# Performance work log

Hardware: AMD Instinct MI355X
Metric: run time of the kernel (lower is better)

Reference implementation:

```python
import jax, jax.numpy as jnp
import numpy as np

B = 1024
E = 512
NUM_HEADS = 8
EPS = 1e-5  # torch LayerNorm default


def _mha(x, w_qkv, b_qkv, w_o, b_o):
    """torch nn.MultiheadAttention (batch_first, self-attn, no dropout).
    x: [N, S, E]; w_qkv: [3E, E]; w_o: [E, E]."""
    N, S, Ex = x.shape
    H = NUM_HEADS
    D = Ex // H
    qkv = x @ w_qkv.T + b_qkv                      # [N, S, 3E]
    q, k, v = jnp.split(qkv, 3, axis=-1)
    q = q.reshape(N, S, H, D).transpose(0, 2, 1, 3)  # [N, H, S, D]
    k = k.reshape(N, S, H, D).transpose(0, 2, 1, 3)
    v = v.reshape(N, S, H, D).transpose(0, 2, 1, 3)
    scores = jnp.einsum('nhqd,nhkd->nhqk', q, k) * (D ** -0.5)
    attn = jax.nn.softmax(scores, axis=-1)
    out = jnp.einsum('nhqk,nhkd->nhqd', attn, v)
    out = out.transpose(0, 2, 1, 3).reshape(N, S, Ex)
    return out @ w_o.T + b_o


def _box_perm(g):
    """Permute 9x9 grid so each 3x3 box becomes a contiguous row of 9.
    This permutation is its own inverse. g: [B, 9, 9, E]."""
    Bx = g.shape[0]
    return (g.reshape(Bx, 3, 3, 3, 3, E)
             .transpose(0, 1, 3, 2, 4, 5)
             .reshape(Bx, 9, 9, E))


def setup_inputs() -> dict:
    key = jax.random.key(0)
    ks = jax.random.split(key, 16)
    s = 0.02
    inp = {'x': jax.random.normal(ks[0], (B, 81, E), jnp.float32)}
    for i, p in enumerate(['row', 'col', 'box']):
        inp[p + '_wqkv'] = jax.random.normal(ks[1 + 2 * i], (3 * E, E), jnp.float32) * s
        inp[p + '_bqkv'] = jnp.zeros((3 * E,), jnp.float32)
        inp[p + '_wo'] = jax.random.normal(ks[2 + 2 * i], (E, E), jnp.float32) * s
        inp[p + '_bo'] = jnp.zeros((E,), jnp.float32)
    inp['w1'] = jax.random.normal(ks[7], (2 * E, 3 * E), jnp.float32) * s
    inp['b1'] = jnp.zeros((2 * E,), jnp.float32)
    inp['w2'] = jax.random.normal(ks[8], (E, 2 * E), jnp.float32) * s
    inp['b2'] = jnp.zeros((E,), jnp.float32)
    inp['gamma'] = jnp.ones((E,), jnp.float32)
    inp['beta'] = jnp.zeros((E,), jnp.float32)
    return inp


def reference(x, row_wqkv, row_bqkv, row_wo, row_bo,
              col_wqkv, col_bqkv, col_wo, col_bo,
              box_wqkv, box_bqkv, box_wo, box_bo,
              w1, b1, w2, b2, gamma, beta):
    Bx = x.shape[0]
    # Row attention: rows are already contiguous groups of 9.
    row_out = _mha(x.reshape(Bx * 9, 9, E), row_wqkv, row_bqkv, row_wo, row_bo)
    row_out = row_out.reshape(Bx, 81, E)
    # Column attention: transpose grid so columns are contiguous.
    col_x = x.reshape(Bx, 9, 9, E).transpose(0, 2, 1, 3).reshape(Bx * 9, 9, E)
    col_out = _mha(col_x, col_wqkv, col_bqkv, col_wo, col_bo)
    col_out = col_out.reshape(Bx, 9, 9, E).transpose(0, 2, 1, 3).reshape(Bx, 81, E)
    # Box attention: permute grid so each 3x3 box is contiguous.
    box_x = _box_perm(x.reshape(Bx, 9, 9, E)).reshape(Bx * 9, 9, E)
    box_out = _mha(box_x, box_wqkv, box_bqkv, box_wo, box_bo)
    box_out = _box_perm(box_out.reshape(Bx, 9, 9, E)).reshape(Bx, 81, E)
    # Constraint mixer MLP.
    combined = jnp.concatenate([row_out, col_out, box_out], axis=-1)  # [B,81,3E]
    h = jax.nn.gelu(combined @ w1.T + b1, approximate=False)
    mixed = h @ w2.T + b2
    # Residual + LayerNorm.
    y = x + mixed
    mu = jnp.mean(y, axis=-1, keepdims=True)
    var = jnp.var(y, axis=-1, keepdims=True)
    return (y - mu) * jax.lax.rsqrt(var + EPS) * gamma + beta
```

## Files before the change

### kernel.cpp

```cpp
#include <hip/hip_runtime.h>
#include <hip/hip_bf16.h>
#include <math.h>

typedef __hip_bfloat16 bf16;
typedef __attribute__((ext_vector_type(8))) short s8v;
typedef __attribute__((ext_vector_type(4))) short s4v;
typedef __attribute__((ext_vector_type(4))) float f4v;

static __device__ __forceinline__ float bfs2f(short s) {
    return __uint_as_float(((unsigned)(unsigned short)s) << 16);
}
static __device__ __forceinline__ short f2bfs(float f) {
    __hip_bfloat16 h = __float2bfloat16(f);
    return *reinterpret_cast<short*>(&h);
}

__global__ __launch_bounds__(256)
void cvt_f32_bf16(const float* __restrict__ in, bf16* __restrict__ out, long n4)
{
    const long i = (long)blockIdx.x * 256 + threadIdx.x;
    if (i >= n4) return;
    const float4 v = reinterpret_cast<const float4*>(in)[i];
    s4v o;
    o[0] = f2bfs(v.x); o[1] = f2bfs(v.y); o[2] = f2bfs(v.z); o[3] = f2bfs(v.w);
    reinterpret_cast<s4v*>(out)[i] = o;
}

__global__ __launch_bounds__(256)
void cvt_t_f32_bf16(const float* __restrict__ in, bf16* __restrict__ out,
                    int R, int C)
{
    __shared__ float t[32][33];
    const int bx = blockIdx.x * 32;
    const int by = blockIdx.y * 32;
    const int tx = threadIdx.x & 31;
    const int ty = threadIdx.x >> 5;
#pragma unroll
    for (int r = ty; r < 32; r += 8)
        t[r][tx] = in[(long)(by + r) * C + bx + tx];
    __syncthreads();
#pragma unroll
    for (int r = ty; r < 32; r += 8)
        out[(long)(bx + r) * R + by + tx] = __float2bfloat16(t[tx][r]);
}

__global__ __launch_bounds__(256)
void fold_b1(const float* __restrict__ w1, const float* __restrict__ bo0,
             const float* __restrict__ bo1, const float* __restrict__ bo2,
             const float* __restrict__ b1, float* __restrict__ b1p)
{
    const int m = blockIdx.x * 256 + threadIdx.x;
    float s = b1[m];
    const float* w = w1 + (long)m * 1536;
    for (int k = 0; k < 512; ++k) s += w[k]        * bo0[k];
    for (int k = 0; k < 512; ++k) s += w[512 + k]  * bo1[k];
    for (int k = 0; k < 512; ++k) s += w[1024 + k] * bo2[k];
    b1p[m] = s;
}

template<int ACT>
__global__ __launch_bounds__(512, 2)
void gemm256(const bf16* __restrict__ A, const bf16* __restrict__ B,
             const float* __restrict__ bias, bf16* __restrict__ C,
             int K, int lda, int ldc, int coff)
{
    __shared__ __align__(16) bf16 sA[2][256 * 64];
    __shared__ __align__(16) bf16 sB[2][256 * 64];
    const int tid  = threadIdx.x;
    const int lane = tid & 63;
    const int wid  = tid >> 6;
    const int nwg  = gridDim.x * gridDim.y;
    const int orig = blockIdx.x + gridDim.x * blockIdx.y;
    const int q = nwg >> 3, r = nwg & 7, xcd = orig & 7;
    const int sb = (xcd < r ? xcd * (q + 1) : r * (q + 1) + (xcd - r) * q) + (orig >> 3);
    const int bCol = sb % gridDim.x;
    const int bRow = sb / gridDim.x;

    const int wr  = (wid >> 2) * 128;
    const int wc  = (wid & 3) * 64;
    const int fr  = lane & 15;
    const int hi4 = lane >> 4;
    const int rx  = fr & 7;

    f4v acc[8][4];
#pragma unroll
    for (int i = 0; i < 8; ++i)
#pragma unroll
        for (int j = 0; j < 4; ++j) acc[i][j] = (f4v)(0.0f);

    const int srow = tid >> 3;
    const int scol = ((tid & 7) ^ (srow & 7)) * 8;
    const bf16* Abase = A + (long)(bRow * 256 + srow) * lda + scol;
    const bf16* Bbase = B + (long)(bCol * 256 + srow) * K + scol;

#define GL16(src, dst)                                                          \
    __builtin_amdgcn_global_load_lds(                                           \
        (const __attribute__((address_space(1))) unsigned int*)(src),           \
        (__attribute__((address_space(3))) unsigned int*)(dst), 16, 0, 0)

#define STAGE_A(h, tt, bc) do {                                                 \
    const bf16* g_ = Abase + (long)(h) * 128 * lda + (long)(tt) * 64;           \
    char* d_ = (char*)sA[bc] + (h) * 16384 + tid * 16;                          \
    GL16(g_, d_); GL16(g_ + 64 * (long)lda, d_ + 8192); } while (0)

#define STAGE_B(h, tt, bc) do {                                                 \
    const bf16* g_ = Bbase + (long)(h) * 128 * K + (long)(tt) * 64;             \
    char* d_ = (char*)sB[bc] + (h) * 16384 + tid * 16;                          \
    GL16(g_, d_); GL16(g_ + 64 * (long)K, d_ + 8192); } while (0)

    const int nk = K >> 6;

    STAGE_A(0, 0, 0); STAGE_A(1, 0, 0);
    STAGE_B(0, 0, 0); STAGE_B(1, 0, 0);
    STAGE_B(0, 1, 1); STAGE_B(1, 1, 1);
    asm volatile("s_waitcnt vmcnt(4)" ::: "memory");
    __builtin_amdgcn_s_barrier();
    __builtin_amdgcn_sched_barrier(0);

    for (int t = 0; t < nk; ++t) {
        const int c = t & 1;
        const char* sAc = (const char*)sA[c];
        const char* sBc = (const char*)sB[c];
        s8v bfr[4][2];
#pragma unroll
        for (int p = 0; p < 4; ++p) {
            s8v afr[2][2];
#pragma unroll
            for (int m2 = 0; m2 < 2; ++m2)
#pragma unroll
                for (int kk = 0; kk < 2; ++kk)
                    afr[m2][kk] = *(const s8v*)(sAc
                        + (wr + (2 * p + m2) * 16 + fr) * 128
                        + (((kk * 4 + hi4) ^ rx) << 4));
            if (p == 0) {
#pragma unroll
                for (int ni = 0; ni < 4; ++ni)
#pragma unroll
                    for (int kk = 0; kk < 2; ++kk)
                        bfr[ni][kk] = *(const s8v*)(sBc
                            + (wc + ni * 16 + fr) * 128
                            + (((kk * 4 + hi4) ^ rx) << 4));
            }
            if (p == 0 && t + 1 < nk) STAGE_A(0, t + 1, c ^ 1);
            if (p == 1 && t + 1 < nk) STAGE_A(1, t + 1, c ^ 1);
            if (p == 2 && t + 2 < nk) STAGE_B(0, t + 2, c);
            if (p == 3 && t + 2 < nk) STAGE_B(1, t + 2, c);

            __builtin_amdgcn_s_barrier();
            asm volatile("s_waitcnt lgkmcnt(0)" ::: "memory");
            __builtin_amdgcn_sched_barrier(0);
            __builtin_amdgcn_s_setprio(1);
#pragma unroll
            for (int kk = 0; kk < 2; ++kk)
#pragma unroll
                for (int m2 = 0; m2 < 2; ++m2)
#pragma unroll
                    for (int ni = 0; ni < 4; ++ni)
                        acc[2 * p + m2][ni] = __builtin_amdgcn_mfma_f32_16x16x32_bf16(
                            afr[m2][kk], bfr[ni][kk], acc[2 * p + m2][ni], 0, 0, 0);
            __builtin_amdgcn_s_setprio(0);
            __builtin_amdgcn_sched_barrier(0);
            if (p == 3) {
                if (t + 2 < nk) {
                    asm volatile("s_waitcnt vmcnt(4)" ::: "memory");
                } else if (t + 1 < nk) {
                    asm volatile("s_waitcnt vmcnt(0)" ::: "memory");
                }
            }
            __builtin_amdgcn_s_barrier();
            __builtin_amdgcn_sched_barrier(0);
        }
    }
#undef STAGE_A
#undef STAGE_B
#undef GL16

    const int frow = hi4 * 4;
    const long rowBase = (long)bRow * 256 + wr;
    const int  colBase = bCol * 256 + wc;
#pragma unroll
    for (int ni = 0; ni < 4; ++ni) {
        const int col = colBase + ni * 16 + fr;
        const float bi = bias ? bias[coff + col] : 0.0f;
#pragma unroll
        for (int mi = 0; mi < 8; ++mi) {
#pragma unroll
            for (int j = 0; j < 4; ++j) {
                float v = acc[mi][ni][j] + bi;
                if (ACT == 1) {
                    const float u = v * (0.7978845608f + 0.0356774081f * v * v);
                    const float tnh = 1.0f - 2.0f / (__expf(2.0f * u) + 1.0f);
                    v = 0.5f * v * (1.0f + tnh);
                }
                const long rr = rowBase + mi * 16 + frow + j;
                C[rr * (long)ldc + coff + col] = __float2bfloat16(v);
            }
        }
    }
}

__global__ __launch_bounds__(256)
void attn9(const bf16* __restrict__ qkv, bf16* __restrict__ outg,
           long chunk_base)
{
    __shared__ __align__(16) bf16 sQKV[9 * 1536];
    __shared__ float sP[8 * 81];
    __shared__ int sTok[9];
    const int tid = threadIdx.x;
    const int branch = blockIdx.y;
    const int bx = blockIdx.x;
    const int s = (bx & 7) * (2304 >> 3) + (bx >> 3);
    const int b = s / 9, g = s % 9;

    if (tid < 9) {
        const int p = tid;
        int cell;
        if (branch == 0)      cell = g * 9 + p;
        else if (branch == 1) cell = p * 9 + g;
        else                  cell = ((g / 3) * 3 + p / 3) * 9 + (g % 3) * 3 + (p % 3);
        sTok[p] = b * 81 + cell;
    }
    __syncthreads();

    const long brOff = (long)branch * 1536;
    for (int c = tid; c < 1728; c += 256) {
        const int p = c / 192;
        const int off = (c - p * 192) * 8;
        *(s8v*)(&sQKV[p * 1536 + off]) =
            *(const s8v*)(&qkv[(long)sTok[p] * 4608 + brOff + off]);
    }
    __syncthreads();

    for (int t = tid; t < 648; t += 256) {
        const int h = t / 81;
        const int r = t - h * 81;
        const int i = r / 9, j = r - (r / 9) * 9;
        const bf16* qp = &sQKV[i * 1536 + h * 64];
        const bf16* kp = &sQKV[j * 1536 + 512 + h * 64];
        float accd = 0.0f;
#pragma unroll
        for (int dc = 0; dc < 8; ++dc) {
            s8v qv = *(const s8v*)(qp + dc * 8);
            s8v kv = *(const s8v*)(kp + dc * 8);
#pragma unroll
            for (int e2 = 0; e2 < 8; ++e2)
                accd += bfs2f(qv[e2]) * bfs2f(kv[e2]);
        }
        sP[t] = accd * 0.125f;
    }
    __syncthreads();

    if (tid < 72) {
        float* row = &sP[tid * 9];
        float m = row[0];
#pragma unroll
        for (int j = 1; j < 9; ++j) m = fmaxf(m, row[j]);
        float sum = 0.f, e[9];
#pragma unroll
        for (int j = 0; j < 9; ++j) { e[j] = expf(row[j] - m); sum += e[j]; }
        const float inv = 1.0f / sum;
#pragma unroll
        for (int j = 0; j < 9; ++j) row[j] = e[j] * inv;
    }
    __syncthreads();

    for (int t = tid; t < 576; t += 256) {
        const int i = t >> 6;
        const int c8 = (t & 63) * 8;
        const int h = (t & 63) >> 3;
        const float* prow = &sP[h * 81 + i * 9];
        float accv[8];
#pragma unroll
        for (int q2 = 0; q2 < 8; ++q2) accv[q2] = 0.f;
#pragma unroll
        for (int j = 0; j < 9; ++j) {
            const float p = prow[j];
            s8v vv = *(const s8v*)(&sQKV[j * 1536 + 1024 + c8]);
#pragma unroll
            for (int q2 = 0; q2 < 8; ++q2)
                accv[q2] += p * bfs2f(vv[q2]);
        }
        s8v ov;
#pragma unroll
        for (int q2 = 0; q2 < 8; ++q2) ov[q2] = f2bfs(accv[q2]);
        *(s8v*)(&outg[(chunk_base + sTok[i]) * 1536 + branch * 512 + c8]) = ov;
    }
}

__global__ __launch_bounds__(256)
void ln_res(const float* __restrict__ x, const bf16* __restrict__ mixed,
            const float* __restrict__ gamma, const float* __restrict__ beta,
            float* __restrict__ out)
{
    const int tid = threadIdx.x;
    const int lane = tid & 63;
    const long row = (long)blockIdx.x * 4 + (tid >> 6);
    const long base = row * 512 + lane * 8;
    const float4 x0 = *(const float4*)(&x[base]);
    const float4 x1 = *(const float4*)(&x[base + 4]);
    const s8v mv = *(const s8v*)(&mixed[base]);
    float y[8];
    y[0] = x0.x + bfs2f(mv[0]); y[1] = x0.y + bfs2f(mv[1]);
    y[2] = x0.z + bfs2f(mv[2]); y[3] = x0.w + bfs2f(mv[3]);
    y[4] = x1.x + bfs2f(mv[4]); y[5] = x1.y + bfs2f(mv[5]);
    y[6] = x1.z + bfs2f(mv[6]); y[7] = x1.w + bfs2f(mv[7]);
    float sum = 0.f, sq = 0.f;
#pragma unroll
    for (int j = 0; j < 8; ++j) { sum += y[j]; sq += y[j] * y[j]; }
#pragma unroll
    for (int o = 32; o > 0; o >>= 1) {
        sum += __shfl_xor(sum, o, 64);
        sq  += __shfl_xor(sq, o, 64);
    }
    const float mean = sum * (1.f / 512.f);
    const float inv = rsqrtf(sq * (1.f / 512.f) - mean * mean + 1e-5f);
    const float4 g0 = *(const float4*)(&gamma[lane * 8]);
    const float4 g1 = *(const float4*)(&gamma[lane * 8 + 4]);
    const float4 b0 = *(const float4*)(&beta[lane * 8]);
    const float4 b1 = *(const float4*)(&beta[lane * 8 + 4]);
    float4 o0, o1;
    o0.x = (y[0] - mean) * inv * g0.x + b0.x;
    o0.y = (y[1] - mean) * inv * g0.y + b0.y;
    o0.z = (y[2] - mean) * inv * g0.z + b0.z;
    o0.w = (y[3] - mean) * inv * g0.w + b0.w;
    o1.x = (y[4] - mean) * inv * g1.x + b1.x;
    o1.y = (y[5] - mean) * inv * g1.y + b1.y;
    o1.z = (y[6] - mean) * inv * g1.z + b1.z;
    o1.w = (y[7] - mean) * inv * g1.w + b1.w;
    *(float4*)(&out[base]) = o0;
    *(float4*)(&out[base + 4]) = o1;
}

extern "C" void kernel_launch(void* const* d_in, const int* in_sizes, int n_in,
                              void* d_out, int out_size, void* d_ws, size_t ws_size,
                              hipStream_t stream)
{
    (void)in_sizes; (void)n_in; (void)out_size; (void)ws_size;
    const float* x     = (const float*)d_in[0];
    const float* w1f   = (const float*)d_in[13];
    const float* b1f   = (const float*)d_in[14];
    const float* b2f   = (const float*)d_in[16];
    const float* gamma = (const float*)d_in[17];
    const float* beta  = (const float*)d_in[18];

    char* ws = (char*)d_ws;
    bf16* attnall   = (bf16*)(ws);
    bf16* mixed     = (bf16*)(ws);
    char* R         = ws + 254803968LL;
    bf16* qkv3chunk = (bf16*)(R);
    bf16* xb        = (bf16*)(R + 191102976LL);
    bf16* h         = (bf16*)(R);
    char* wb        = ws + 530841600LL;
    long off = 0;
    bf16* wqkv3_b = (bf16*)(wb + off); off += 4718592;
    bf16* woT_b[3];
    for (int i = 0; i < 3; ++i) { woT_b[i] = (bf16*)(wb + off); off += 524288; }
    bf16* w1_b  = (bf16*)(wb + off); off += 3145728;
    bf16* w2_b  = (bf16*)(wb + off); off += 1048576;
    bf16* Wp    = (bf16*)(wb + off); off += 3145728;
    float* b1p  = (float*)(wb + off); off += 4096;
    float* bqkv3 = (float*)(wb + off); off += 18432;

    const dim3 blk(256, 1, 1);
    const dim3 blk512(512, 1, 1);

    cvt_f32_bf16<<<dim3(41472), blk, 0, stream>>>(x, xb, 10616832L);
    for (int i = 0; i < 3; ++i) {
        cvt_f32_bf16<<<dim3(768), blk, 0, stream>>>(
            (const float*)d_in[1 + i * 4], wqkv3_b + (long)i * 786432, 196608L);
        cvt_t_f32_bf16<<<dim3(16, 16), blk, 0, stream>>>(
            (const float*)d_in[3 + i * 4], woT_b[i], 512, 512);
        hipMemcpyAsync(bqkv3 + i * 1536, d_in[2 + i * 4], 1536 * sizeof(float),
                       hipMemcpyDeviceToDevice, stream);
    }
    cvt_f32_bf16<<<dim3(1536), blk, 0, stream>>>(w1f, w1_b, 393216L);
    cvt_f32_bf16<<<dim3(512), blk, 0, stream>>>((const float*)d_in[15], w2_b, 131072L);

    fold_b1<<<dim3(4), blk, 0, stream>>>(w1f, (const float*)d_in[4],
                                         (const float*)d_in[8], (const float*)d_in[12],
                                         b1f, b1p);

    for (int br = 0; br < 3; ++br)
        gemm256<0><<<dim3(2, 4), blk512, 0, stream>>>(
            w1_b + br * 512, woT_b[br], nullptr, Wp, 512, 1536, 1536, br * 512);

    const long ROWS_C = 20736;
    for (int c = 0; c < 4; ++c) {
        const bf16* xA = xb + c * ROWS_C * 512;
        gemm256<0><<<dim3(18, 81), blk512, 0, stream>>>(
            xA, wqkv3_b, bqkv3, qkv3chunk, 512, 512, 4608, 0);
        attn9<<<dim3(2304, 3), blk, 0, stream>>>(qkv3chunk, attnall, c * ROWS_C);
    }
    gemm256<1><<<dim3(4, 324), blk512, 0, stream>>>(attnall, Wp, b1p, h, 1536, 1536, 1024, 0);
    gemm256<0><<<dim3(2, 324), blk512, 0, stream>>>(h, w2_b, b2f, mixed, 1024, 1024, 512, 0);
    ln_res<<<dim3(20736), blk, 0, stream>>>(x, mixed, gamma, beta, (float*)d_out);
}
```

Before: 1.727 ms.

## Restructure GEMM K-loop into two phases with fewer barriers and explicit waits

Each K step of the bf16 MFMA GEMM main loop now runs in two phases instead of four, each covering half the M fragments. The per-phase barriers, lgkmcnt waits and sched_barriers are removed, so the compiler schedules the LDS reads and MFMAs freely. The intent is to cut synchronisation overhead and let LDS loads overlap with matrix math. The trade-off is more live fragment registers and reliance on compiler-inserted waits, which could raise register pressure or add hazards around the async global-to-LDS staging.

```diff
diff --git a/kernel.cpp b/kernel.cpp
--- a/kernel.cpp
+++ b/kernel.cpp
@@ -108,6 +108,9 @@
     char* d_ = (char*)sB[bc] + (h) * 16384 + tid * 16;                          \
     GL16(g_, d_); GL16(g_ + 64 * (long)K, d_ + 8192); } while (0)
 
+#define LDSW(base, row, kk)                                                     \
+    (*(const s8v*)((base) + (row) * 128 + ((((kk) * 4 + hi4) ^ rx) << 4)))
+
     const int nk = K >> 6;
 
     STAGE_A(0, 0, 0); STAGE_A(1, 0, 0);
@@ -122,58 +125,74 @@
         const char* sAc = (const char*)sA[c];
         const char* sBc = (const char*)sB[c];
         s8v bfr[4][2];
-#pragma unroll
-        for (int p = 0; p < 4; ++p) {
-            s8v afr[2][2];
+
+        {
+            s8v af0[2][2], af1[2][2];
 #pragma unroll
             for (int m2 = 0; m2 < 2; ++m2)
 #pragma unroll
+                for (int kk = 0; kk < 2; ++kk) {
+                    af0[m2][kk] = LDSW(sAc, wr + m2 * 16 + fr, kk);
+                    af1[m2][kk] = LDSW(sAc, wr + (2 + m2) * 16 + fr, kk);
+                }
+#pragma unroll
+            for (int ni = 0; ni < 4; ++ni)
+#pragma unroll
                 for (int kk = 0; kk < 2; ++kk)
-                    afr[m2][kk] = *(const s8v*)(sAc
-                        + (wr + (2 * p + m2) * 16 + fr) * 128
-                        + (((kk * 4 + hi4) ^ rx) << 4));
-            if (p == 0) {
-#pragma unroll
-                for (int ni = 0; ni < 4; ++ni)
-#pragma unroll
-                    for (int kk = 0; kk < 2; ++kk)
-                        bfr[ni][kk] = *(const s8v*)(sBc
-                            + (wc + ni * 16 + fr) * 128
-                            + (((kk * 4 + hi4) ^ rx) << 4));
-            }
-            if (p == 0 && t + 1 < nk) STAGE_A(0, t + 1, c ^ 1);
-            if (p == 1 && t + 1 < nk) STAGE_A(1, t + 1, c ^ 1);
-            if (p == 2 && t + 2 < nk) STAGE_B(0, t + 2, c);
-            if (p == 3 && t + 2 < nk) STAGE_B(1, t + 2, c);
-
-            __builtin_amdgcn_s_barrier();
-            asm volatile("s_waitcnt lgkmcnt(0)" ::: "memory");
-            __builtin_amdgcn_sched_barrier(0);
+                    bfr[ni][kk] = LDSW(sBc, wc + ni * 16 + fr, kk);
+            if (t + 1 < nk) { STAGE_A(0, t + 1, c ^ 1); STAGE_A(1, t + 1, c ^ 1); }
             __builtin_amdgcn_s_setprio(1);
 #pragma unroll
             for (int kk = 0; kk < 2; ++kk)
 #pragma unroll
                 for (int m2 = 0; m2 < 2; ++m2)
 #pragma unroll
-                    for (int ni = 0; ni < 4; ++ni)
-                        acc[2 * p + m2][ni] = __builtin_amdgcn_mfma_f32_16x16x32_bf16(
-                            afr[m2][kk], bfr[ni][kk], acc[2 * p + m2][ni], 0, 0, 0);
+                    for (int ni = 0; ni < 4; ++ni) {
+                        acc[m2][ni] = __builtin_amdgcn_mfma_f32_16x16x32_bf16(
+                            af0[m2][kk], bfr[ni][kk], acc[m2][ni], 0, 0, 0);
+                        acc[2 + m2][ni] = __builtin_amdgcn_mfma_f32_16x16x32_bf16(
+                            af1[m2][kk], bfr[ni][kk], acc[2 + m2][ni], 0, 0, 0);
+                    }
             __builtin_amdgcn_s_setprio(0);
-            __builtin_amdgcn_sched_barrier(0);
-            if (p == 3) {
-                if (t + 2 < nk) {
-                    asm volatile("s_waitcnt vmcnt(4)" ::: "memory");
-                } else if (t + 1 < nk) {
-                    asm volatile("s_waitcnt vmcnt(0)" ::: "memory");
+        }
+        __builtin_amdgcn_s_barrier();
+
+        {
+            s8v af0[2][2], af1[2][2];
+#pragma unroll
+            for (int m2 = 0; m2 < 2; ++m2)
+#pragma unroll
+                for (int kk = 0; kk < 2; ++kk) {
+                    af0[m2][kk] = LDSW(sAc, wr + (4 + m2) * 16 + fr, kk);
+                    af1[m2][kk] = LDSW(sAc, wr + (6 + m2) * 16 + fr, kk);
                 }
-            }
-            __builtin_amdgcn_s_barrier();
-            __builtin_amdgcn_sched_barrier(0);
-        }
+            if (t + 2 < nk) { STAGE_B(0, t + 2, c); STAGE_B(1, t + 2, c); }
+            __builtin_amdgcn_s_setprio(1);
+#pragma unroll
+            for (int kk = 0; kk < 2; ++kk)
+#pragma unroll
+                for (int m2 = 0; m2 < 2; ++m2)
+#pragma unroll
+                    for (int ni = 0; ni < 4; ++ni) {
+                        acc[4 + m2][ni] = __builtin_amdgcn_mfma_f32_16x16x32_bf16(
+                            af0[m2][kk], bfr[ni][kk], acc[4 + m2][ni], 0, 0, 0);
+                        acc[6 + m2][ni] = __builtin_amdgcn_mfma_f32_16x16x32_bf16(
+                            af1[m2][kk], bfr[ni][kk], acc[6 + m2][ni], 0, 0, 0);
+                    }
+            __builtin_amdgcn_s_setprio(0);
+        }
+        if (t + 2 < nk) {
+            asm volatile("s_waitcnt vmcnt(4)" ::: "memory");
+        } else if (t + 1 < nk) {
+            asm volatile("s_waitcnt vmcnt(0)" ::: "memory");
+        }
+        __builtin_amdgcn_s_barrier();
+        __builtin_amdgcn_sched_barrier(0);
     }
 #undef STAGE_A
 #undef STAGE_B
 #undef GL16
+#undef LDSW
 
     const int frow = hi4 * 4;
     const long rowBase = (long)bRow * 256 + wr;
```

Result: faster. 1.564 ms (-9.4%).

## Simplify GEMM pipeline to one-ahead prefetch and stage epilogue through LDS

Applied to the files above, without the earlier changes.

Replaces the staggered four-phase main loop, which split the A and B prefetches across sub-phases with per-phase barriers, with a simpler loop. It prefetches the entire next K-tile at the top, computes all MFMAs for the current tile, then waits and synchronizes once per iteration. The epilogue now writes bias- and activation-adjusted results into shared memory per warp, then emits coalesced 16-byte row stores to global instead of scattered 2-byte stores. The fewer barriers and coalesced writes aim to cut sync and store overhead, but the loop loses the deeper B prefetch and the finer interleaving of loads with compute.

```diff
diff --git a/kernel.cpp b/kernel.cpp
--- a/kernel.cpp
+++ b/kernel.cpp
@@ -108,65 +108,56 @@
     char* d_ = (char*)sB[bc] + (h) * 16384 + tid * 16;                          \
     GL16(g_, d_); GL16(g_ + 64 * (long)K, d_ + 8192); } while (0)
 
+#define LDSW(base, row, kk)                                                     \
+    (*(const s8v*)((base) + (row) * 128 + ((((kk) * 4 + hi4) ^ rx) << 4)))
+
     const int nk = K >> 6;
 
     STAGE_A(0, 0, 0); STAGE_A(1, 0, 0);
     STAGE_B(0, 0, 0); STAGE_B(1, 0, 0);
-    STAGE_B(0, 1, 1); STAGE_B(1, 1, 1);
-    asm volatile("s_waitcnt vmcnt(4)" ::: "memory");
+    asm volatile("s_waitcnt vmcnt(0)" ::: "memory");
     __builtin_amdgcn_s_barrier();
-    __builtin_amdgcn_sched_barrier(0);
 
     for (int t = 0; t < nk; ++t) {
         const int c = t & 1;
         const char* sAc = (const char*)sA[c];
         const char* sBc = (const char*)sB[c];
+
+        if (t + 1 < nk) {
+            STAGE_A(0, t + 1, c ^ 1); STAGE_A(1, t + 1, c ^ 1);
+            STAGE_B(0, t + 1, c ^ 1); STAGE_B(1, t + 1, c ^ 1);
+        }
+
         s8v bfr[4][2];
 #pragma unroll
-        for (int p = 0; p < 4; ++p) {
-            s8v afr[2][2];
-#pragma unroll
-            for (int m2 = 0; m2 < 2; ++m2)
-#pragma unroll
-                for (int kk = 0; kk < 2; ++kk)
-                    afr[m2][kk] = *(const s8v*)(sAc
-                        + (wr + (2 * p + m2) * 16 + fr) * 128
-                        + (((kk * 4 + hi4) ^ rx) << 4));
-            if (p == 0) {
-#pragma unroll
-                for (int ni = 0; ni < 4; ++ni)
-#pragma unroll
-                    for (int kk = 0; kk < 2; ++kk)
-                        bfr[ni][kk] = *(const s8v*)(sBc
-                            + (wc + ni * 16 + fr) * 128
-                            + (((kk * 4 + hi4) ^ rx) << 4));
+        for (int ni = 0; ni < 4; ++ni)
+#pragma unroll
+            for (int kk = 0; kk < 2; ++kk)
+                bfr[ni][kk] = LDSW(sBc, wc + ni * 16 + fr, kk);
+
+#pragma unroll
+        for (int g = 0; g < 4; ++g) {
+            s8v a0[2], a1[2];
+#pragma unroll
+            for (int kk = 0; kk < 2; ++kk) {
+                a0[kk] = LDSW(sAc, wr + (2 * g) * 16 + fr, kk);
+                a1[kk] = LDSW(sAc, wr + (2 * g + 1) * 16 + fr, kk);
             }
-            if (p == 0 && t + 1 < nk) STAGE_A(0, t + 1, c ^ 1);
-            if (p == 1 && t + 1 < nk) STAGE_A(1, t + 1, c ^ 1);
-            if (p == 2 && t + 2 < nk) STAGE_B(0, t + 2, c);
-            if (p == 3 && t + 2 < nk) STAGE_B(1, t + 2, c);
-
-            __builtin_amdgcn_s_barrier();
-            asm volatile("s_waitcnt lgkmcnt(0)" ::: "memory");
-            __builtin_amdgcn_sched_barrier(0);
             __builtin_amdgcn_s_setprio(1);
 #pragma unroll
             for (int kk = 0; kk < 2; ++kk)
 #pragma unroll
-                for (int m2 = 0; m2 < 2; ++m2)
-#pragma unroll
-                    for (int ni = 0; ni < 4; ++ni)
-                        acc[2 * p + m2][ni] = __builtin_amdgcn_mfma_f32_16x16x32_bf16(
-                            afr[m2][kk], bfr[ni][kk], acc[2 * p + m2][ni], 0, 0, 0);
+                for (int ni = 0; ni < 4; ++ni) {
+                    acc[2 * g][ni] = __builtin_amdgcn_mfma_f32_16x16x32_bf16(
+                        a0[kk], bfr[ni][kk], acc[2 * g][ni], 0, 0, 0);
+                    acc[2 * g + 1][ni] = __builtin_amdgcn_mfma_f32_16x16x32_bf16(
+                        a1[kk], bfr[ni][kk], acc[2 * g + 1][ni], 0, 0, 0);
+                }
             __builtin_amdgcn_s_setprio(0);
-            __builtin_amdgcn_sched_barrier(0);
-            if (p == 3) {
-                if (t + 2 < nk) {
-                    asm volatile("s_waitcnt vmcnt(4)" ::: "memory");
-                } else if (t + 1 < nk) {
-                    asm volatile("s_waitcnt vmcnt(0)" ::: "memory");
-                }
-            }
+        }
+
+        if (t + 1 < nk) {
+            asm volatile("s_waitcnt vmcnt(0)" ::: "memory");
             __builtin_amdgcn_s_barrier();
             __builtin_amdgcn_sched_barrier(0);
         }
@@ -174,7 +165,11 @@
 #undef STAGE_A
 #undef STAGE_B
 #undef GL16
-
+#undef LDSW
+
+    __syncthreads();
+    bf16* ep = (wid < 4) ? ((bf16*)sA + wid * 8192)
+                         : ((bf16*)sB + (wid - 4) * 8192);
     const int frow = hi4 * 4;
     const long rowBase = (long)bRow * 256 + wr;
     const int  colBase = bCol * 256 + wc;
@@ -192,10 +187,19 @@
                     const float tnh = 1.0f - 2.0f / (__expf(2.0f * u) + 1.0f);
                     v = 0.5f * v * (1.0f + tnh);
                 }
-                const long rr = rowBase + mi * 16 + frow + j;
-                C[rr * (long)ldc + coff + col] = __float2bfloat16(v);
+                ep[(mi * 16 + frow + j) * 64 + ni * 16 + fr] = __float2bfloat16(v);
             }
         }
+    }
+    asm volatile("s_waitcnt lgkmcnt(0)" ::: "memory");
+    __builtin_amdgcn_sched_barrier(0);
+    const int lr8 = lane >> 3;
+    const int lc  = (lane & 7) * 8;
+#pragma unroll
+    for (int q2 = 0; q2 < 16; ++q2) {
+        const int lrow = q2 * 8 + lr8;
+        const s8v vv = *(const s8v*)(&ep[lrow * 64 + lc]);
+        *(s8v*)(&C[(rowBase + lrow) * (long)ldc + coff + colBase + lc]) = vv;
     }
 }
 
```

After: 1.667 ms. 1.04x faster.
